# Kernel optimization log

Hardware: AMD Instinct MI355X
Metric: run time of the kernel (lower is better)

## Reference

```python
import jax, jax.numpy as jnp
import numpy as np

B, T, W, D = 4, 1000, 32, 200
ED, N, DCONV, DTR = 400, 16, 4, 13  # d_inner=2*d_model, d_state, d_conv, dt_rank=ceil(200/16)


def _causal_conv(x, w, b):
    # x: (B, L, ED), depthwise causal conv, kernel DCONV
    L = x.shape[1]
    xp = jnp.pad(x, ((0, 0), (DCONV - 1, 0), (0, 0)))
    y = sum(xp[:, k:k + L, :] * w[:, k] for k in range(DCONV))
    return y + b


def _ssm(x, A_log, Dp, xproj, dtw, dtb):
    # selective scan; x: (B, L, ED)
    A = -jnp.exp(A_log)                      # (ED, N)
    dbc = x @ xproj                          # (B, L, DTR+2N)
    delta, Bm, Cm = dbc[..., :DTR], dbc[..., DTR:DTR + N], dbc[..., DTR + N:]
    dt = jax.nn.softplus(delta @ dtw + dtb)  # (B, L, ED)
    dA = jnp.exp(dt[..., None] * A)                         # (B, L, ED, N)
    dBx = dt[..., None] * Bm[:, :, None, :] * x[..., None]  # (B, L, ED, N)

    def step(h, t):
        dA_t, dBx_t, C_t = t
        h = dA_t * h + dBx_t
        y = jnp.einsum('ben,bn->be', h, C_t)
        return h, y

    h0 = jnp.zeros((x.shape[0], ED, N), x.dtype)
    xs = (dA.transpose(1, 0, 2, 3), dBx.transpose(1, 0, 2, 3), Cm.transpose(1, 0, 2))
    _, ys = jax.lax.scan(step, h0, xs)
    return ys.transpose(1, 0, 2) + Dp * x


def _branch(x, in_proj, conv_w, conv_b, xproj, dtw, dtb, A_log, Dp):
    xz = x @ in_proj
    xp, z = xz[..., :ED], xz[..., ED:]
    xp = jax.nn.silu(_causal_conv(xp, conv_w, conv_b))
    y = _ssm(xp, A_log, Dp, xproj, dtw, dtb)
    return y * jax.nn.silu(z)


def setup_inputs() -> dict:
    key = jax.random.key(0)
    ks = jax.random.split(key, 24)
    s = 0.02
    nrm = lambda k, shape: jax.random.normal(k, shape, jnp.float32) * s
    inp = {}
    inp['input_ids'] = jax.random.normal(ks[0], (B, T, W, D), jnp.float32)
    inp['n_tweets'] = jax.random.randint(ks[1], (B,), 1, T + 1)
    inp['n_words'] = jax.random.randint(ks[2], (B, T), 1, W + 1)
    inp['cls_token'] = jnp.zeros((1, 1, D), jnp.float32)
    inp['w_attn'] = nrm(ks[3], (D, 1))
    inp['b_attn'] = jnp.zeros((1,), jnp.float32)
    inp['norm_w'] = jnp.ones((D,), jnp.float32)
    for i, d in enumerate(('f', 'b')):
        o = i * 8
        inp[f'in_proj_{d}'] = nrm(ks[4 + o], (D, 2 * ED))
        inp[f'conv_w_{d}'] = nrm(ks[5 + o], (ED, DCONV))
        inp[f'conv_b_{d}'] = jnp.zeros((ED,), jnp.float32)
        inp[f'xproj_{d}'] = nrm(ks[6 + o], (ED, DTR + 2 * N))
        inp[f'dtw_{d}'] = nrm(ks[7 + o], (DTR, ED))
        inp[f'dtb_{d}'] = jnp.zeros((ED,), jnp.float32)
        inp[f'A_log_{d}'] = jnp.log(jnp.broadcast_to(jnp.arange(1, N + 1, dtype=jnp.float32), (ED, N)))
        inp[f'D_{d}'] = jnp.ones((ED,), jnp.float32)
    inp['out_proj'] = nrm(ks[20], (ED, D))
    inp['head_w'] = nrm(ks[21], (D, 1))
    inp['head_b'] = jnp.zeros((1,), jnp.float32)
    return inp


def reference(input_ids, n_tweets, n_words, cls_token, w_attn, b_attn, norm_w,
              in_proj_f, conv_w_f, conv_b_f, xproj_f, dtw_f, dtb_f, A_log_f, D_f,
              in_proj_b, conv_w_b, conv_b_b, xproj_b, dtw_b, dtb_b, A_log_b, D_b,
              out_proj, head_w, head_b):
    Bz, Tz, Wz, Dz = input_ids.shape
    # ragged per-tweet attention pooling, fully vectorized with masks
    scores = jnp.squeeze(input_ids @ w_attn, -1) + b_attn[0]        # (B, T, W)
    wmask = jnp.arange(Wz) < n_words[..., None]                     # (B, T, W)
    scores = jnp.where(wmask, scores, -jnp.inf)
    attn = jax.nn.softmax(scores, axis=-1)
    tw = jnp.einsum('btw,btwd->btd', attn, input_ids)               # (B, T, D)
    tmask = jnp.arange(Tz) < n_tweets[:, None]
    tw = jnp.where(tmask[..., None], tw, 0.0)                       # padded tweets stay zero
    pos = Tz // 2
    x = jnp.concatenate([tw[:, :pos], jnp.broadcast_to(cls_token, (Bz, 1, Dz)), tw[:, pos:]], axis=1)
    # one bidirectional Mamba layer: pre-RMSNorm residual block
    xn = x * jax.lax.rsqrt(jnp.mean(x * x, axis=-1, keepdims=True) + 1e-5) * norm_w
    y_f = _branch(xn, in_proj_f, conv_w_f, conv_b_f, xproj_f, dtw_f, dtb_f, A_log_f, D_f)
    y_b = jnp.flip(_branch(jnp.flip(xn, 1), in_proj_b, conv_w_b, conv_b_b, xproj_b, dtw_b, dtb_b, A_log_b, D_b), 1)
    x = x + (y_f + y_b) @ out_proj
    logit = jnp.squeeze(x[:, pos] @ head_w, -1) + head_b[0]
    return jax.nn.sigmoid(logit)
```

## Files before the change

kernel.cpp:

```cpp
#include <hip/hip_runtime.h>
#include <cmath>

#define Bz 4
#define Tz 1000
#define Wz 32
#define Dz 200
#define EDz 400
#define Nz 16
#define DTRz 13
#define Lz 1001
#define POSz 500
#define LPz 501
#define TSTR 512
#define ESP 10
#define NEG_BIG -1e30f

__device__ __forceinline__ float wave_sum(float v) {
#pragma unroll
  for (int o = 32; o; o >>= 1) v += __shfl_xor(v, o);
  return v;
}

__global__ __launch_bounds__(256) void k_front(
    const float* __restrict__ x, const int* __restrict__ n_tweets,
    const int* __restrict__ n_words, const float* __restrict__ w_attn,
    const float* __restrict__ b_attn, const float* __restrict__ norm_w,
    const float* __restrict__ cls, const float* __restrict__ out_proj,
    const float* __restrict__ head_w, const float* __restrict__ ipf,
    const float* __restrict__ ipb, float* __restrict__ xn,
    float* __restrict__ zbuf, float* __restrict__ vbuf) {
  int bid = blockIdx.x;
  int tid = threadIdx.x;
  int wave = tid >> 6, lane = tid & 63;
  if (bid < 9) {
    if (bid == 0) {
      __shared__ float hw[Dz];
      if (tid < Dz) hw[tid] = head_w[tid];
      __syncthreads();
      for (int e = tid; e < EDz; e += 256) {
        float acc = 0.f;
        for (int d = 0; d < Dz; d += 4) {
          float4 ov = *(const float4*)(out_proj + e * Dz + d);
          acc += ov.x * hw[d] + ov.y * hw[d + 1] + ov.z * hw[d + 2] + ov.w * hw[d + 3];
        }
        vbuf[e] = acc;
      }
      return;
    }
    int id = bid - 1;
    int br = id >> 2, b = id & 3;
    __shared__ float xs[Dz];
    __shared__ float s_red[4];
    float val = (tid < Dz) ? cls[tid] : 0.f;
    float sq = wave_sum(val * val);
    if ((tid & 63) == 0) s_red[tid >> 6] = sq;
    __syncthreads();
    float tot = s_red[0] + s_red[1] + s_red[2] + s_red[3];
    float scale = rsqrtf(tot * (1.f / Dz) + 1e-5f);
    if (tid < Dz) {
      float o = val * scale * norm_w[tid];
      xs[tid] = o;
      if (br == 0) xn[((size_t)b * Lz + POSz) * Dz + tid] = o;
    }
    __syncthreads();
    const float* ip = br ? ipb : ipf;
    for (int e = tid; e < EDz; e += 256) {
      float acc = 0.f;
      for (int d = 0; d < Dz; ++d) acc += xs[d] * ip[d * (2 * EDz) + EDz + e];
      zbuf[((size_t)br * Bz + b) * EDz + e] = acc;
    }
    return;
  }
  int bt = (bid - 9) * 4 + wave;
  int b = bt / Tz, t = bt - b * Tz;
  int l = (t < POSz) ? t : t + 1;
  float* outr = xn + ((size_t)b * Lz + l) * Dz;
  int ntw = n_tweets[b]; if (ntw > Tz) ntw = Tz;
  if (t >= ntw) {
    if (lane < 50) *(float4*)(outr + lane * 4) = make_float4(0.f, 0.f, 0.f, 0.f);
    return;
  }
  int nw = n_words[b * Tz + t]; if (nw > Wz) nw = Wz; if (nw < 1) nw = 1;
  const float* xs = x + ((size_t)(b * Tz + t)) * (Wz * Dz);
  int h = lane & 1, w = lane >> 1;
  float sc = 0.f;
  if (w < nw) {
    const float* xr = xs + w * Dz + h * 100;
    const float* wr = w_attn + h * 100;
#pragma unroll
    for (int i = 0; i < 25; ++i) {
      float4 xv = *(const float4*)(xr + i * 4);
      float4 wv = *(const float4*)(wr + i * 4);
      sc += xv.x * wv.x + xv.y * wv.y + xv.z * wv.z + xv.w * wv.w;
    }
  }
  sc += __shfl_xor(sc, 1);
  float scv = (w < nw) ? (sc + b_attn[0]) : NEG_BIG;
  float m = scv;
#pragma unroll
  for (int o = 32; o; o >>= 1) m = fmaxf(m, __shfl_xor(m, o));
  float en = __expf(scv - m);
  float es = (h == 0) ? en : 0.f;
  float tot = wave_sum(es);
  en /= tot;
  float4 val = make_float4(0.f, 0.f, 0.f, 0.f);
  const float* xc = xs + lane * 4;
  for (int ww = 0; ww < nw; ++ww) {
    float aw = __shfl(en, 2 * ww);
    if (lane < 50) {
      float4 xv = *(const float4*)(xc + ww * Dz);
      val.x += aw * xv.x; val.y += aw * xv.y;
      val.z += aw * xv.z; val.w += aw * xv.w;
    }
  }
  float sq = (lane < 50) ? (val.x * val.x + val.y * val.y + val.z * val.z + val.w * val.w) : 0.f;
  sq = wave_sum(sq);
  float scale = rsqrtf(sq * (1.f / Dz) + 1e-5f);
  if (lane < 50) {
    float4 nw4 = *(const float4*)(norm_w + lane * 4);
    float4 o = make_float4(val.x * scale * nw4.x, val.y * scale * nw4.y,
                           val.z * scale * nw4.z, val.w * scale * nw4.w);
    *(float4*)(outr + lane * 4) = o;
  }
}

__global__ __launch_bounds__(256) void k_gemm(
    const float* __restrict__ xn, const float* __restrict__ ipf,
    const float* __restrict__ ipb, float* __restrict__ P) {
  int bid = blockIdx.x;
  int brb = bid / 56;
  int rr = bid - brb * 56;
  int tt = rr / 7, ee = rr - tt * 7;
  int br = brb >> 2, b = brb & 3;
  int t0 = tt * 64, e0 = ee * 64;
  const float* ip = br ? ipb : ipf;
  int tid = threadIdx.x;
  int tx = tid & 15, ty = tid >> 4;

  __shared__ float Xs[16][64 + 4];
  __shared__ float Ws[16][64 + 4];

  float acc[4][4];
#pragma unroll
  for (int i = 0; i < 4; ++i)
#pragma unroll
    for (int j = 0; j < 4; ++j) acc[i][j] = 0.f;

  int xr = tid >> 2, xc = (tid & 3) * 4;
  int wr = tid >> 4, wc = (tid & 15) * 4;
  int t = t0 + xr;
  bool tok = (t < LPz);
  int l = br ? (Lz - 1 - t) : t;
  const float* xrow = xn + ((size_t)b * Lz + l) * Dz;

  for (int dk = 0; dk < 200; dk += 16) {
    float xv[4], wv[4];
#pragma unroll
    for (int c = 0; c < 4; ++c) {
      int d = dk + xc + c;
      xv[c] = (tok && d < Dz) ? xrow[d] : 0.f;
    }
    int dw = dk + wr;
#pragma unroll
    for (int c = 0; c < 4; ++c) {
      int e = e0 + wc + c;
      wv[c] = (dw < Dz && e < EDz) ? ip[(size_t)dw * (2 * EDz) + e] : 0.f;
    }
    __syncthreads();
#pragma unroll
    for (int c = 0; c < 4; ++c) Xs[xc + c][xr] = xv[c];
#pragma unroll
    for (int c = 0; c < 4; ++c) Ws[wr][wc + c] = wv[c];
    __syncthreads();
#pragma unroll
    for (int k = 0; k < 16; ++k) {
      float4 a4 = *(const float4*)&Xs[k][ty * 4];
      float4 b4 = *(const float4*)&Ws[k][tx * 4];
      float av[4] = {a4.x, a4.y, a4.z, a4.w};
      float bv[4] = {b4.x, b4.y, b4.z, b4.w};
#pragma unroll
      for (int i = 0; i < 4; ++i)
#pragma unroll
        for (int j = 0; j < 4; ++j) acc[i][j] += av[i] * bv[j];
    }
  }
#pragma unroll
  for (int j = 0; j < 4; ++j) {
    int e = e0 + tx * 4 + j;
    if (e < EDz) {
      float4 o = make_float4(acc[0][j], acc[1][j], acc[2][j], acc[3][j]);
      *(float4*)&P[((size_t)brb * EDz + e) * TSTR + t0 + ty * 4] = o;
    }
  }
}

__global__ __launch_bounds__(256) void k_mid(
    const float* __restrict__ P,
    const float* __restrict__ cwf, const float* __restrict__ cwb,
    const float* __restrict__ cbf, const float* __restrict__ cbb,
    const float* __restrict__ xpjf, const float* __restrict__ xpjb,
    float* __restrict__ xp_t, float* __restrict__ dbcp) {
  int bid = blockIdx.x;
  int esp = bid % ESP;
  int rem = bid / ESP;
  int tc = rem & 7, brb = rem >> 3;
  int br = brb >> 2;
  int tid = threadIdx.x;
  int wave = tid >> 6, lane = tid & 63;
  int t = tc * 64 + lane;
  const float* cw = br ? cwb : cwf;
  const float* cb = br ? cbb : cbf;
  const float* xpj = br ? xpjb : xpjf;

  __shared__ float sred[4][64][45];

  float accq[45];
#pragma unroll
  for (int q = 0; q < 45; ++q) accq[q] = 0.f;

  const float* Pb = P + (size_t)brb * EDz * TSTR;
  int e0 = esp * 40 + wave * 10;
#pragma unroll 2
  for (int i = 0; i < 10; ++i) {
    int e = e0 + i;
    const float* pr = Pb + (size_t)e * TSTR;
    float p0 = (t >= 3) ? pr[t - 3] : 0.f;
    float p1 = (t >= 2) ? pr[t - 2] : 0.f;
    float p2 = (t >= 1) ? pr[t - 1] : 0.f;
    float p3 = pr[t];
    float4 c4 = *(const float4*)(cw + e * 4);
    float a = cb[e] + c4.x * p0 + c4.y * p1 + c4.z * p2 + c4.w * p3;
    float sp = a / (1.f + __expf(-a));
    xp_t[((size_t)brb * EDz + e) * TSTR + t] = sp;
    const float* xq = xpj + e * 45;
#pragma unroll
    for (int q = 0; q < 45; ++q) accq[q] += sp * xq[q];
  }
#pragma unroll
  for (int q = 0; q < 45; ++q) sred[wave][lane][q] = accq[q];
  __syncthreads();
  if (wave < 2) {
#pragma unroll
    for (int q = 0; q < 45; ++q)
      sred[wave][lane][q] += sred[wave + 2][lane][q];
  }
  __syncthreads();
  if (wave == 0) {
    float* dp = dbcp + ((size_t)(esp * 8 + brb) * 45) * TSTR + t;
#pragma unroll
    for (int q = 0; q < 45; ++q)
      dp[(size_t)q * TSTR] = sred[0][lane][q] + sred[1][lane][q];
  }
}

__global__ __launch_bounds__(256) void k_dt2(
    const float* __restrict__ dbcp,
    const float* __restrict__ dtwf, const float* __restrict__ dtwb,
    const float* __restrict__ dtbf, const float* __restrict__ dtbb,
    float* __restrict__ dt_t, float* __restrict__ Bm_t,
    float* __restrict__ Cend) {
  int bid = blockIdx.x;
  int egrp = bid % 11;
  int rem = bid / 11;
  int tc = rem & 7, brb = rem >> 3;
  int br = brb >> 2;
  int tid = threadIdx.x;
  int wave = tid >> 6, lane = tid & 63;
  int t = tc * 64 + lane;
  const size_t espstr = (size_t)8 * 45 * TSTR;

  if (egrp == 10) {
    for (int idx = tid; idx < 16 * 64; idx += 256) {
      int n = idx >> 6, tl = idx & 63;
      size_t base = ((size_t)brb * 45 + 13 + n) * TSTR + tc * 64 + tl;
      float s = 0.f;
#pragma unroll
      for (int esp = 0; esp < ESP; ++esp) s += dbcp[base + esp * espstr];
      Bm_t[((size_t)brb * Nz + n) * TSTR + tc * 64 + tl] = s;
    }
    if (tc == 7 && tid < Nz) {
      size_t base = ((size_t)brb * 45 + 29 + tid) * TSTR + POSz;
      float s = 0.f;
#pragma unroll
      for (int esp = 0; esp < ESP; ++esp) s += dbcp[base + esp * espstr];
      Cend[brb * Nz + tid] = s;
    }
    return;
  }

  __shared__ float dfin[DTRz][64];
  for (int idx = tid; idx < DTRz * 64; idx += 256) {
    int q = idx >> 6, tl = idx & 63;
    size_t base = ((size_t)brb * 45 + q) * TSTR + tc * 64 + tl;
    float s = 0.f;
#pragma unroll
    for (int esp = 0; esp < ESP; ++esp) s += dbcp[base + esp * espstr];
    dfin[q][tl] = s;
  }
  __syncthreads();
  const float* dtw = br ? dtwb : dtwf;
  const float* dtb = br ? dtbb : dtbf;
  float dq[DTRz];
#pragma unroll
  for (int q = 0; q < DTRz; ++q) dq[q] = dfin[q][lane];
  int e0 = egrp * 40 + wave * 10;
#pragma unroll 2
  for (int i = 0; i < 10; ++i) {
    int e = e0 + i;
    float s = dtb[e];
#pragma unroll
    for (int q = 0; q < DTRz; ++q) s += dq[q] * dtw[q * EDz + e];
    float dtv = (s > 20.f) ? s : log1pf(__expf(s));
    dt_t[((size_t)brb * EDz + e) * TSTR + t] = dtv;
  }
}

__global__ __launch_bounds__(64) void k_scan(
    const float* __restrict__ xp_t, const float* __restrict__ dt_t,
    const float* __restrict__ Bm_t, const float* __restrict__ Cend,
    const float* __restrict__ Alogf, const float* __restrict__ Alogb,
    const float* __restrict__ Dpf, const float* __restrict__ Dpb,
    const float* __restrict__ zbuf, const float* __restrict__ vbuf,
    float* __restrict__ ybuf) {
  int blk = blockIdx.x;
  int br = blk / (Bz * EDz);
  int rem = blk - br * (Bz * EDz);
  int b = rem / EDz, e = rem - b * EDz;
  int lane = threadIdx.x;
  const float* A_log = br ? Alogb : Alogf;
  const float* Dp = br ? Dpb : Dpf;
  float A[Nz];
  {
    const float4* ap = (const float4*)(A_log + e * Nz);
#pragma unroll
    for (int q = 0; q < 4; ++q) {
      float4 a4 = ap[q];
      A[q * 4 + 0] = -__expf(a4.x); A[q * 4 + 1] = -__expf(a4.y);
      A[q * 4 + 2] = -__expf(a4.z); A[q * 4 + 3] = -__expf(a4.w);
    }
  }
  size_t base = ((size_t)(br * Bz + b) * EDz + e) * TSTR;
  const float* dtp = dt_t + base;
  const float* xpp = xp_t + base;
  const float* bmp = Bm_t + (size_t)(br * Bz + b) * Nz * TSTR;
  float loc = 0.f;
#pragma unroll
  for (int c = 0; c < 8; ++c) {
    int t = c * 64 + lane;
    if (t < LPz) loc += dtp[t];
  }
  float Stot = wave_sum(loc);
  float acc[Nz];
#pragma unroll
  for (int n = 0; n < Nz; ++n) acc[n] = 0.f;
  float carry = 0.f;
  for (int c = 0; c < 8; ++c) {
    int t = c * 64 + lane;
    bool act = t < LPz;
    float dtt = 0.f, xv = 0.f;
    if (act) { dtt = dtp[t]; xv = xpp[t]; }
    float s = dtt;
#pragma unroll
    for (int o = 1; o < 64; o <<= 1) {
      float u = __shfl_up(s, o);
      s += (lane >= o) ? u : 0.f;
    }
    float S = carry + s;
    carry += __shfl(s, 63);
    float wt = dtt * xv;
    float decay = Stot - S;
#pragma unroll
    for (int n = 0; n < Nz; ++n) {
      float bv = 0.f;
      if (act) bv = bmp[n * TSTR + t];
      acc[n] += __expf(A[n] * decay) * wt * bv;
    }
  }
#pragma unroll
  for (int o = 32; o; o >>= 1) {
#pragma unroll
    for (int n = 0; n < Nz; ++n) acc[n] += __shfl_xor(acc[n], o);
  }
  if (lane == 0) {
    float y = Dp[e] * xpp[LPz - 1];
#pragma unroll
    for (int n = 0; n < Nz; ++n) y += Cend[(br * Bz + b) * Nz + n] * acc[n];
    float zz = zbuf[((size_t)br * Bz + b) * EDz + e];
    float sz = zz / (1.f + __expf(-zz));
    ybuf[((size_t)br * Bz + b) * EDz + e] = y * sz * vbuf[e];
  }
}

__global__ __launch_bounds__(256) void k_final(
    const float* __restrict__ cls, const float* __restrict__ head_w,
    const float* __restrict__ head_b, const float* __restrict__ ybuf,
    float* __restrict__ out) {
  int tid = threadIdx.x;
  int b = tid >> 6, lane = tid & 63;
  float acc = 0.f;
  for (int e = lane; e < EDz; e += 64)
    acc += ybuf[(size_t)b * EDz + e] + ybuf[(size_t)(Bz + b) * EDz + e];
  for (int d = lane; d < Dz; d += 64) acc += cls[d] * head_w[d];
  acc = wave_sum(acc);
  if (lane == 0) out[b] = 1.f / (1.f + __expf(-(acc + head_b[0])));
}

extern "C" void kernel_launch(void* const* d_in, const int* in_sizes, int n_in,
                              void* d_out, int out_size, void* d_ws, size_t ws_size,
                              hipStream_t stream) {
  const float* input_ids = (const float*)d_in[0];
  const int* n_tweets = (const int*)d_in[1];
  const int* n_words = (const int*)d_in[2];
  const float* cls = (const float*)d_in[3];
  const float* w_attn = (const float*)d_in[4];
  const float* b_attn = (const float*)d_in[5];
  const float* norm_w = (const float*)d_in[6];
  const float* ip[2] = {(const float*)d_in[7], (const float*)d_in[15]};
  const float* cw[2] = {(const float*)d_in[8], (const float*)d_in[16]};
  const float* cb[2] = {(const float*)d_in[9], (const float*)d_in[17]};
  const float* xpj[2] = {(const float*)d_in[10], (const float*)d_in[18]};
  const float* dtw[2] = {(const float*)d_in[11], (const float*)d_in[19]};
  const float* dtbp[2] = {(const float*)d_in[12], (const float*)d_in[20]};
  const float* Alog[2] = {(const float*)d_in[13], (const float*)d_in[21]};
  const float* Dpp[2] = {(const float*)d_in[14], (const float*)d_in[22]};
  const float* out_proj = (const float*)d_in[23];
  const float* head_w = (const float*)d_in[24];
  const float* head_b = (const float*)d_in[25];
  float* out = (float*)d_out;

  float* ws = (float*)d_ws;
  float* xn = ws;
  float* Pbuf = xn + 800800;
  float* xp_t = Pbuf + 1638400;
  float* dt_t = xp_t + 1638400;
  float* Bm_t = dt_t + 1638400;
  float* dbcp = Bm_t + 65536;
  float* Cend = dbcp + 1843200;
  float* zbuf = Cend + 128;
  float* vbuf = zbuf + 3200;
  float* ybuf = vbuf + 400;

  hipLaunchKernelGGL(k_front, dim3(9 + Bz * Tz / 4), dim3(256), 0, stream,
                     input_ids, n_tweets, n_words, w_attn, b_attn, norm_w,
                     cls, out_proj, head_w, ip[0], ip[1], xn, zbuf, vbuf);
  hipLaunchKernelGGL(k_gemm, dim3(2 * Bz * 8 * 7), dim3(256), 0, stream,
                     xn, ip[0], ip[1], Pbuf);
  hipLaunchKernelGGL(k_mid, dim3(2 * Bz * 8 * ESP), dim3(256), 0, stream,
                     Pbuf, cw[0], cw[1], cb[0], cb[1], xpj[0], xpj[1],
                     xp_t, dbcp);
  hipLaunchKernelGGL(k_dt2, dim3(2 * Bz * 8 * 11), dim3(256), 0, stream,
                     dbcp, dtw[0], dtw[1], dtbp[0], dtbp[1],
                     dt_t, Bm_t, Cend);
  hipLaunchKernelGGL(k_scan, dim3(2 * Bz * EDz), dim3(64), 0, stream,
                     xp_t, dt_t, Bm_t, Cend, Alog[0], Alog[1], Dpp[0], Dpp[1],
                     zbuf, vbuf, ybuf);
  hipLaunchKernelGGL(k_final, dim3(1), dim3(256), 0, stream,
                     cls, head_w, head_b, ybuf, out);
}
```

Measured before the change: 107.4 us.

## Fuse dt projection into mid kernel and final reduction into scan via atomic counters

Removes two kernel launches by using last-block-done atomic counters. The k_dt2 work (reducing the split-E partial dbc, softplus dt projection, Bm and Cend) now runs in whichever k_mid2 block finishes last for its (branch, batch, time-chunk) tile. The k_final head reduction now runs in the last k_scan2 block. This saves launch and sync overhead, but the dt projection is serialised onto 64 tail blocks, each looping over all 400 channels, where it was spread across 704 blocks before, which may lengthen the tail.

```diff
diff --git a/kernel.cpp b/kernel.cpp
--- a/kernel.cpp
+++ b/kernel.cpp
@@ -28,12 +28,14 @@
     const float* __restrict__ cls, const float* __restrict__ out_proj,
     const float* __restrict__ head_w, const float* __restrict__ ipf,
     const float* __restrict__ ipb, float* __restrict__ xn,
-    float* __restrict__ zbuf, float* __restrict__ vbuf) {
+    float* __restrict__ zbuf, float* __restrict__ vbuf,
+    int* __restrict__ cnts) {
   int bid = blockIdx.x;
   int tid = threadIdx.x;
   int wave = tid >> 6, lane = tid & 63;
   if (bid < 9) {
     if (bid == 0) {
+      if (tid < 72) cnts[tid] = 0;
       __shared__ float hw[Dz];
       if (tid < Dz) hw[tid] = head_w[tid];
       __syncthreads();
@@ -194,12 +196,16 @@
   }
 }
 
-__global__ __launch_bounds__(256) void k_mid(
+__global__ __launch_bounds__(256) void k_mid2(
     const float* __restrict__ P,
     const float* __restrict__ cwf, const float* __restrict__ cwb,
     const float* __restrict__ cbf, const float* __restrict__ cbb,
     const float* __restrict__ xpjf, const float* __restrict__ xpjb,
-    float* __restrict__ xp_t, float* __restrict__ dbcp) {
+    const float* __restrict__ dtwf, const float* __restrict__ dtwb,
+    const float* __restrict__ dtbf, const float* __restrict__ dtbb,
+    float* __restrict__ xp_t, float* __restrict__ dbcp,
+    float* __restrict__ dt_t, float* __restrict__ Bm_t,
+    float* __restrict__ Cend, int* __restrict__ cnts) {
   int bid = blockIdx.x;
   int esp = bid % ESP;
   int rem = bid / ESP;
@@ -213,6 +219,8 @@
   const float* xpj = br ? xpjb : xpjf;
 
   __shared__ float sred[4][64][45];
+  __shared__ float dfin[DTRz * 64];
+  __shared__ int s_last;
 
   float accq[45];
 #pragma unroll
@@ -251,62 +259,50 @@
     for (int q = 0; q < 45; ++q)
       dp[(size_t)q * TSTR] = sred[0][lane][q] + sred[1][lane][q];
   }
-}
-
-__global__ __launch_bounds__(256) void k_dt2(
-    const float* __restrict__ dbcp,
-    const float* __restrict__ dtwf, const float* __restrict__ dtwb,
-    const float* __restrict__ dtbf, const float* __restrict__ dtbb,
-    float* __restrict__ dt_t, float* __restrict__ Bm_t,
-    float* __restrict__ Cend) {
-  int bid = blockIdx.x;
-  int egrp = bid % 11;
-  int rem = bid / 11;
-  int tc = rem & 7, brb = rem >> 3;
-  int br = brb >> 2;
-  int tid = threadIdx.x;
-  int wave = tid >> 6, lane = tid & 63;
-  int t = tc * 64 + lane;
+  __syncthreads();
+  __threadfence();
+  if (tid == 0) {
+    int old = atomicAdd(&cnts[brb * 8 + tc], 1);
+    s_last = (old == ESP - 1) ? 1 : 0;
+  }
+  __syncthreads();
+  if (!s_last) return;
+  __threadfence();
+
   const size_t espstr = (size_t)8 * 45 * TSTR;
-
-  if (egrp == 10) {
-    for (int idx = tid; idx < 16 * 64; idx += 256) {
-      int n = idx >> 6, tl = idx & 63;
-      size_t base = ((size_t)brb * 45 + 13 + n) * TSTR + tc * 64 + tl;
-      float s = 0.f;
-#pragma unroll
-      for (int esp = 0; esp < ESP; ++esp) s += dbcp[base + esp * espstr];
-      Bm_t[((size_t)brb * Nz + n) * TSTR + tc * 64 + tl] = s;
-    }
-    if (tc == 7 && tid < Nz) {
-      size_t base = ((size_t)brb * 45 + 29 + tid) * TSTR + POSz;
-      float s = 0.f;
-#pragma unroll
-      for (int esp = 0; esp < ESP; ++esp) s += dbcp[base + esp * espstr];
-      Cend[brb * Nz + tid] = s;
-    }
-    return;
-  }
-
-  __shared__ float dfin[DTRz][64];
   for (int idx = tid; idx < DTRz * 64; idx += 256) {
     int q = idx >> 6, tl = idx & 63;
     size_t base = ((size_t)brb * 45 + q) * TSTR + tc * 64 + tl;
     float s = 0.f;
 #pragma unroll
-    for (int esp = 0; esp < ESP; ++esp) s += dbcp[base + esp * espstr];
-    dfin[q][tl] = s;
+    for (int e2 = 0; e2 < ESP; ++e2) s += dbcp[base + e2 * espstr];
+    dfin[q * 64 + tl] = s;
+  }
+  for (int idx = tid; idx < Nz * 64; idx += 256) {
+    int n = idx >> 6, tl = idx & 63;
+    size_t base = ((size_t)brb * 45 + 13 + n) * TSTR + tc * 64 + tl;
+    float s = 0.f;
+#pragma unroll
+    for (int e2 = 0; e2 < ESP; ++e2) s += dbcp[base + e2 * espstr];
+    Bm_t[((size_t)brb * Nz + n) * TSTR + tc * 64 + tl] = s;
+  }
+  if (tc == 7 && tid < Nz) {
+    size_t base = ((size_t)brb * 45 + 29 + tid) * TSTR + POSz;
+    float s = 0.f;
+#pragma unroll
+    for (int e2 = 0; e2 < ESP; ++e2) s += dbcp[base + e2 * espstr];
+    Cend[brb * Nz + tid] = s;
   }
   __syncthreads();
   const float* dtw = br ? dtwb : dtwf;
   const float* dtb = br ? dtbb : dtbf;
   float dq[DTRz];
 #pragma unroll
-  for (int q = 0; q < DTRz; ++q) dq[q] = dfin[q][lane];
-  int e0 = egrp * 40 + wave * 10;
+  for (int q = 0; q < DTRz; ++q) dq[q] = dfin[q * 64 + lane];
+  int ew0 = wave * 100;
 #pragma unroll 2
-  for (int i = 0; i < 10; ++i) {
-    int e = e0 + i;
+  for (int i = 0; i < 100; ++i) {
+    int e = ew0 + i;
     float s = dtb[e];
 #pragma unroll
     for (int q = 0; q < DTRz; ++q) s += dq[q] * dtw[q * EDz + e];
@@ -315,13 +311,15 @@
   }
 }
 
-__global__ __launch_bounds__(64) void k_scan(
+__global__ __launch_bounds__(64) void k_scan2(
     const float* __restrict__ xp_t, const float* __restrict__ dt_t,
     const float* __restrict__ Bm_t, const float* __restrict__ Cend,
     const float* __restrict__ Alogf, const float* __restrict__ Alogb,
     const float* __restrict__ Dpf, const float* __restrict__ Dpb,
     const float* __restrict__ zbuf, const float* __restrict__ vbuf,
-    float* __restrict__ ybuf) {
+    float* __restrict__ ybuf, const float* __restrict__ cls,
+    const float* __restrict__ head_w, const float* __restrict__ head_b,
+    float* __restrict__ out, int* __restrict__ cnt) {
   int blk = blockIdx.x;
   int br = blk / (Bz * EDz);
   int rem = blk - br * (Bz * EDz);
@@ -389,20 +387,22 @@
     float sz = zz / (1.f + __expf(-zz));
     ybuf[((size_t)br * Bz + b) * EDz + e] = y * sz * vbuf[e];
   }
-}
-
-__global__ __launch_bounds__(256) void k_final(
-    const float* __restrict__ cls, const float* __restrict__ head_w,
-    const float* __restrict__ head_b, const float* __restrict__ ybuf,
-    float* __restrict__ out) {
-  int tid = threadIdx.x;
-  int b = tid >> 6, lane = tid & 63;
-  float acc = 0.f;
-  for (int e = lane; e < EDz; e += 64)
-    acc += ybuf[(size_t)b * EDz + e] + ybuf[(size_t)(Bz + b) * EDz + e];
-  for (int d = lane; d < Dz; d += 64) acc += cls[d] * head_w[d];
-  acc = wave_sum(acc);
-  if (lane == 0) out[b] = 1.f / (1.f + __expf(-(acc + head_b[0])));
+  __threadfence();
+  int old = 0;
+  if (lane == 0) old = atomicAdd(cnt, 1);
+  old = __shfl(old, 0);
+  if (old != 2 * Bz * EDz - 1) return;
+  __threadfence();
+  float ch = 0.f;
+  for (int d = lane; d < Dz; d += 64) ch += cls[d] * head_w[d];
+  ch = wave_sum(ch) + head_b[0];
+  for (int b2 = 0; b2 < Bz; ++b2) {
+    float a2 = 0.f;
+    for (int e2 = lane; e2 < EDz; e2 += 64)
+      a2 += ybuf[(size_t)b2 * EDz + e2] + ybuf[(size_t)(Bz + b2) * EDz + e2];
+    a2 = wave_sum(a2);
+    if (lane == 0) out[b2] = 1.f / (1.f + __expf(-(a2 + ch)));
+  }
 }
 
 extern "C" void kernel_launch(void* const* d_in, const int* in_sizes, int n_in,
@@ -439,21 +439,18 @@
   float* zbuf = Cend + 128;
   float* vbuf = zbuf + 3200;
   float* ybuf = vbuf + 400;
+  int* cnts = (int*)(ybuf + 3200 + 64);
 
   hipLaunchKernelGGL(k_front, dim3(9 + Bz * Tz / 4), dim3(256), 0, stream,
                      input_ids, n_tweets, n_words, w_attn, b_attn, norm_w,
-                     cls, out_proj, head_w, ip[0], ip[1], xn, zbuf, vbuf);
+                     cls, out_proj, head_w, ip[0], ip[1], xn, zbuf, vbuf, cnts);
   hipLaunchKernelGGL(k_gemm, dim3(2 * Bz * 8 * 7), dim3(256), 0, stream,
                      xn, ip[0], ip[1], Pbuf);
-  hipLaunchKernelGGL(k_mid, dim3(2 * Bz * 8 * ESP), dim3(256), 0, stream,
+  hipLaunchKernelGGL(k_mid2, dim3(2 * Bz * 8 * ESP), dim3(256), 0, stream,
                      Pbuf, cw[0], cw[1], cb[0], cb[1], xpj[0], xpj[1],
-                     xp_t, dbcp);
-  hipLaunchKernelGGL(k_dt2, dim3(2 * Bz * 8 * 11), dim3(256), 0, stream,
-                     dbcp, dtw[0], dtw[1], dtbp[0], dtbp[1],
-                     dt_t, Bm_t, Cend);
-  hipLaunchKernelGGL(k_scan, dim3(2 * Bz * EDz), dim3(64), 0, stream,
+                     dtw[0], dtw[1], dtbp[0], dtbp[1],
+                     xp_t, dbcp, dt_t, Bm_t, Cend, cnts);
+  hipLaunchKernelGGL(k_scan2, dim3(2 * Bz * EDz), dim3(64), 0, stream,
                      xp_t, dt_t, Bm_t, Cend, Alog[0], Alog[1], Dpp[0], Dpp[1],
-                     zbuf, vbuf, ybuf);
-  hipLaunchKernelGGL(k_final, dim3(1), dim3(256), 0, stream,
-                     cls, head_w, head_b, ybuf, out);
-}
+                     zbuf, vbuf, ybuf, cls, head_w, head_b, out, cnts + 64);
+}
```

Result: slower. 374.8 us (+249.0%).

## Fuse in_proj GEMM with conv/x_proj and move dt projection into scan

Applied to the files above, without the earlier changes.

Merges the in_proj GEMM with the causal conv, SiLU and x_proj partial-sum stage. Each block computes an 80-row tile that includes an 8-row halo, keeps it in shared memory, and so no longer round-trips the P buffer through global memory. The dt projection and softplus move out of the dt kernel into the scan kernel, which computes them per lane from the reduced delta rows, so the dt_t buffer is never written or read. This removes one launch and a large share of global traffic. In exchange the GEMM recomputes the halo rows, shared memory per block grows (which may lower occupancy), and the scan does extra arithmetic.

```diff
diff --git a/kernel.cpp b/kernel.cpp
--- a/kernel.cpp
+++ b/kernel.cpp
@@ -12,7 +12,7 @@
 #define POSz 500
 #define LPz 501
 #define TSTR 512
-#define ESP 10
+#define NEE 7
 #define NEG_BIG -1e30f
 
 __device__ __forceinline__ float wave_sum(float v) {
@@ -124,117 +124,108 @@
   }
 }
 
-__global__ __launch_bounds__(256) void k_gemm(
-    const float* __restrict__ xn, const float* __restrict__ ipf,
-    const float* __restrict__ ipb, float* __restrict__ P) {
-  int bid = blockIdx.x;
-  int brb = bid / 56;
-  int rr = bid - brb * 56;
-  int tt = rr / 7, ee = rr - tt * 7;
-  int br = brb >> 2, b = brb & 3;
-  int t0 = tt * 64, e0 = ee * 64;
-  const float* ip = br ? ipb : ipf;
-  int tid = threadIdx.x;
-  int tx = tid & 15, ty = tid >> 4;
-
-  __shared__ float Xs[16][64 + 4];
-  __shared__ float Ws[16][64 + 4];
-
-  float acc[4][4];
-#pragma unroll
-  for (int i = 0; i < 4; ++i)
-#pragma unroll
-    for (int j = 0; j < 4; ++j) acc[i][j] = 0.f;
-
-  int xr = tid >> 2, xc = (tid & 3) * 4;
-  int wr = tid >> 4, wc = (tid & 15) * 4;
-  int t = t0 + xr;
-  bool tok = (t < LPz);
-  int l = br ? (Lz - 1 - t) : t;
-  const float* xrow = xn + ((size_t)b * Lz + l) * Dz;
-
-  for (int dk = 0; dk < 200; dk += 16) {
-    float xv[4], wv[4];
-#pragma unroll
-    for (int c = 0; c < 4; ++c) {
-      int d = dk + xc + c;
-      xv[c] = (tok && d < Dz) ? xrow[d] : 0.f;
-    }
-    int dw = dk + wr;
-#pragma unroll
-    for (int c = 0; c < 4; ++c) {
-      int e = e0 + wc + c;
-      wv[c] = (dw < Dz && e < EDz) ? ip[(size_t)dw * (2 * EDz) + e] : 0.f;
-    }
-    __syncthreads();
-#pragma unroll
-    for (int c = 0; c < 4; ++c) Xs[xc + c][xr] = xv[c];
-#pragma unroll
-    for (int c = 0; c < 4; ++c) Ws[wr][wc + c] = wv[c];
-    __syncthreads();
-#pragma unroll
-    for (int k = 0; k < 16; ++k) {
-      float4 a4 = *(const float4*)&Xs[k][ty * 4];
-      float4 b4 = *(const float4*)&Ws[k][tx * 4];
-      float av[4] = {a4.x, a4.y, a4.z, a4.w};
-      float bv[4] = {b4.x, b4.y, b4.z, b4.w};
-#pragma unroll
-      for (int i = 0; i < 4; ++i)
-#pragma unroll
-        for (int j = 0; j < 4; ++j) acc[i][j] += av[i] * bv[j];
-    }
-  }
-#pragma unroll
-  for (int j = 0; j < 4; ++j) {
-    int e = e0 + tx * 4 + j;
-    if (e < EDz) {
-      float4 o = make_float4(acc[0][j], acc[1][j], acc[2][j], acc[3][j]);
-      *(float4*)&P[((size_t)brb * EDz + e) * TSTR + t0 + ty * 4] = o;
-    }
-  }
-}
-
-__global__ __launch_bounds__(256) void k_mid(
-    const float* __restrict__ P,
+__global__ __launch_bounds__(256) void k_gemmid(
+    const float* __restrict__ xn,
+    const float* __restrict__ ipf, const float* __restrict__ ipb,
     const float* __restrict__ cwf, const float* __restrict__ cwb,
     const float* __restrict__ cbf, const float* __restrict__ cbb,
     const float* __restrict__ xpjf, const float* __restrict__ xpjb,
     float* __restrict__ xp_t, float* __restrict__ dbcp) {
   int bid = blockIdx.x;
-  int esp = bid % ESP;
-  int rem = bid / ESP;
-  int tc = rem & 7, brb = rem >> 3;
-  int br = brb >> 2;
+  int ee = bid % NEE;
+  int rem = bid / NEE;
+  int tt = rem & 7, brb = rem >> 3;
+  int br = brb >> 2, b = brb & 3;
+  int t0 = tt * 64, e0 = ee * 64;
   int tid = threadIdx.x;
   int wave = tid >> 6, lane = tid & 63;
-  int t = tc * 64 + lane;
+  const float* ip = br ? ipb : ipf;
   const float* cw = br ? cwb : cwf;
   const float* cb = br ? cbb : cbf;
   const float* xpj = br ? xpjb : xpjf;
 
+  __shared__ float Xs[16][85];
+  __shared__ float Ws[16][68];
+  __shared__ float Pl[80][69];
   __shared__ float sred[4][64][45];
 
+  int tx = tid & 15, ty = tid >> 4;
+  float acc[5][4];
+#pragma unroll
+  for (int i = 0; i < 5; ++i)
+#pragma unroll
+    for (int j = 0; j < 4; ++j) acc[i][j] = 0.f;
+
+  for (int dk = 0; dk < 200; dk += 16) {
+    float xv[5];
+#pragma unroll
+    for (int r = 0; r < 5; ++r) {
+      int trow = r * 16 + ty;
+      int t = t0 - 8 + trow;
+      int d = dk + tx;
+      float v = 0.f;
+      if (t >= 0 && t < LPz && d < Dz) {
+        int l = br ? (Lz - 1 - t) : t;
+        v = xn[((size_t)b * Lz + l) * Dz + d];
+      }
+      xv[r] = v;
+    }
+    int dw = dk + ty;
+    int e4 = e0 + tx * 4;
+    float wv[4];
+#pragma unroll
+    for (int c = 0; c < 4; ++c) {
+      int e = e4 + c;
+      wv[c] = (dw < Dz && e < EDz) ? ip[(size_t)dw * (2 * EDz) + e] : 0.f;
+    }
+    __syncthreads();
+#pragma unroll
+    for (int r = 0; r < 5; ++r) Xs[tx][r * 16 + ty] = xv[r];
+#pragma unroll
+    for (int c = 0; c < 4; ++c) Ws[ty][tx * 4 + c] = wv[c];
+    __syncthreads();
+#pragma unroll
+    for (int k = 0; k < 16; ++k) {
+      float av[5], bv[4];
+#pragma unroll
+      for (int i = 0; i < 5; ++i) av[i] = Xs[k][ty * 5 + i];
+#pragma unroll
+      for (int j = 0; j < 4; ++j) bv[j] = Ws[k][tx * 4 + j];
+#pragma unroll
+      for (int i = 0; i < 5; ++i)
+#pragma unroll
+        for (int j = 0; j < 4; ++j) acc[i][j] += av[i] * bv[j];
+    }
+  }
+  __syncthreads();
+#pragma unroll
+  for (int i = 0; i < 5; ++i)
+#pragma unroll
+    for (int j = 0; j < 4; ++j) Pl[ty * 5 + i][tx * 4 + j] = acc[i][j];
+  __syncthreads();
+
   float accq[45];
 #pragma unroll
   for (int q = 0; q < 45; ++q) accq[q] = 0.f;
-
-  const float* Pb = P + (size_t)brb * EDz * TSTR;
-  int e0 = esp * 40 + wave * 10;
+  int t = t0 + lane;
 #pragma unroll 2
-  for (int i = 0; i < 10; ++i) {
-    int e = e0 + i;
-    const float* pr = Pb + (size_t)e * TSTR;
-    float p0 = (t >= 3) ? pr[t - 3] : 0.f;
-    float p1 = (t >= 2) ? pr[t - 2] : 0.f;
-    float p2 = (t >= 1) ? pr[t - 1] : 0.f;
-    float p3 = pr[t];
-    float4 c4 = *(const float4*)(cw + e * 4);
-    float a = cb[e] + c4.x * p0 + c4.y * p1 + c4.z * p2 + c4.w * p3;
-    float sp = a / (1.f + __expf(-a));
-    xp_t[((size_t)brb * EDz + e) * TSTR + t] = sp;
-    const float* xq = xpj + e * 45;
-#pragma unroll
-    for (int q = 0; q < 45; ++q) accq[q] += sp * xq[q];
+  for (int i = 0; i < 16; ++i) {
+    int e_loc = wave * 16 + i;
+    int e = e0 + e_loc;
+    if (e < EDz) {
+      int row = lane + 8;
+      float p0 = Pl[row - 3][e_loc];
+      float p1 = Pl[row - 2][e_loc];
+      float p2 = Pl[row - 1][e_loc];
+      float p3 = Pl[row][e_loc];
+      float4 c4 = *(const float4*)(cw + e * 4);
+      float a = cb[e] + c4.x * p0 + c4.y * p1 + c4.z * p2 + c4.w * p3;
+      float sp = a / (1.f + __expf(-a));
+      xp_t[((size_t)brb * EDz + e) * TSTR + t] = sp;
+      const float* xq = xpj + e * 45;
+#pragma unroll
+      for (int q = 0; q < 45; ++q) accq[q] += sp * xq[q];
+    }
   }
 #pragma unroll
   for (int q = 0; q < 45; ++q) sred[wave][lane][q] = accq[q];
@@ -246,89 +237,63 @@
   }
   __syncthreads();
   if (wave == 0) {
-    float* dp = dbcp + ((size_t)(esp * 8 + brb) * 45) * TSTR + t;
+    float* dp = dbcp + ((size_t)(ee * 8 + brb) * 45) * TSTR + t;
 #pragma unroll
     for (int q = 0; q < 45; ++q)
       dp[(size_t)q * TSTR] = sred[0][lane][q] + sred[1][lane][q];
   }
 }
 
-__global__ __launch_bounds__(256) void k_dt2(
-    const float* __restrict__ dbcp,
-    const float* __restrict__ dtwf, const float* __restrict__ dtwb,
-    const float* __restrict__ dtbf, const float* __restrict__ dtbb,
-    float* __restrict__ dt_t, float* __restrict__ Bm_t,
-    float* __restrict__ Cend) {
+__global__ __launch_bounds__(256) void k_dt3(
+    const float* __restrict__ dbcp, float* __restrict__ dfin_g,
+    float* __restrict__ Bm_t, float* __restrict__ Cend) {
   int bid = blockIdx.x;
-  int egrp = bid % 11;
-  int rem = bid / 11;
+  int rg = bid & 3;
+  int rem = bid >> 2;
   int tc = rem & 7, brb = rem >> 3;
-  int br = brb >> 2;
   int tid = threadIdx.x;
-  int wave = tid >> 6, lane = tid & 63;
-  int t = tc * 64 + lane;
   const size_t espstr = (size_t)8 * 45 * TSTR;
-
-  if (egrp == 10) {
-    for (int idx = tid; idx < 16 * 64; idx += 256) {
-      int n = idx >> 6, tl = idx & 63;
-      size_t base = ((size_t)brb * 45 + 13 + n) * TSTR + tc * 64 + tl;
-      float s = 0.f;
-#pragma unroll
-      for (int esp = 0; esp < ESP; ++esp) s += dbcp[base + esp * espstr];
-      Bm_t[((size_t)brb * Nz + n) * TSTR + tc * 64 + tl] = s;
-    }
-    if (tc == 7 && tid < Nz) {
-      size_t base = ((size_t)brb * 45 + 29 + tid) * TSTR + POSz;
-      float s = 0.f;
-#pragma unroll
-      for (int esp = 0; esp < ESP; ++esp) s += dbcp[base + esp * espstr];
-      Cend[brb * Nz + tid] = s;
-    }
-    return;
-  }
-
-  __shared__ float dfin[DTRz][64];
-  for (int idx = tid; idx < DTRz * 64; idx += 256) {
-    int q = idx >> 6, tl = idx & 63;
-    size_t base = ((size_t)brb * 45 + q) * TSTR + tc * 64 + tl;
+  int r0 = rg * 8;
+  int nrows = (rg == 3) ? 5 : 8;
+  for (int idx = tid; idx < nrows * 64; idx += 256) {
+    int rl = idx >> 6, tl = idx & 63;
+    int row = r0 + rl;
+    size_t base = ((size_t)brb * 45 + row) * TSTR + tc * 64 + tl;
     float s = 0.f;
 #pragma unroll
-    for (int esp = 0; esp < ESP; ++esp) s += dbcp[base + esp * espstr];
-    dfin[q][tl] = s;
-  }
-  __syncthreads();
-  const float* dtw = br ? dtwb : dtwf;
-  const float* dtb = br ? dtbb : dtbf;
-  float dq[DTRz];
-#pragma unroll
-  for (int q = 0; q < DTRz; ++q) dq[q] = dfin[q][lane];
-  int e0 = egrp * 40 + wave * 10;
-#pragma unroll 2
-  for (int i = 0; i < 10; ++i) {
-    int e = e0 + i;
-    float s = dtb[e];
-#pragma unroll
-    for (int q = 0; q < DTRz; ++q) s += dq[q] * dtw[q * EDz + e];
-    float dtv = (s > 20.f) ? s : log1pf(__expf(s));
-    dt_t[((size_t)brb * EDz + e) * TSTR + t] = dtv;
-  }
-}
-
-__global__ __launch_bounds__(64) void k_scan(
-    const float* __restrict__ xp_t, const float* __restrict__ dt_t,
+    for (int p = 0; p < NEE; ++p) s += dbcp[base + p * espstr];
+    int tg = tc * 64 + tl;
+    if (row < DTRz) dfin_g[((size_t)brb * DTRz + row) * TSTR + tg] = s;
+    else Bm_t[((size_t)brb * Nz + (row - DTRz)) * TSTR + tg] = s;
+  }
+  if (rg == 3 && tc == 7 && tid < Nz) {
+    size_t base = ((size_t)brb * 45 + 29 + tid) * TSTR + POSz;
+    float s = 0.f;
+#pragma unroll
+    for (int p = 0; p < NEE; ++p) s += dbcp[base + p * espstr];
+    Cend[brb * Nz + tid] = s;
+  }
+}
+
+__global__ __launch_bounds__(64) void k_scan3(
+    const float* __restrict__ xp_t, const float* __restrict__ dfin_g,
     const float* __restrict__ Bm_t, const float* __restrict__ Cend,
     const float* __restrict__ Alogf, const float* __restrict__ Alogb,
     const float* __restrict__ Dpf, const float* __restrict__ Dpb,
+    const float* __restrict__ dtwf, const float* __restrict__ dtwb,
+    const float* __restrict__ dtbf, const float* __restrict__ dtbb,
     const float* __restrict__ zbuf, const float* __restrict__ vbuf,
     float* __restrict__ ybuf) {
   int blk = blockIdx.x;
   int br = blk / (Bz * EDz);
   int rem = blk - br * (Bz * EDz);
   int b = rem / EDz, e = rem - b * EDz;
+  int brb = br * Bz + b;
   int lane = threadIdx.x;
   const float* A_log = br ? Alogb : Alogf;
   const float* Dp = br ? Dpb : Dpf;
+  const float* dtw = br ? dtwb : dtwf;
+  const float* dtb = br ? dtbb : dtbf;
   float A[Nz];
   {
     const float4* ap = (const float4*)(A_log + e * Nz);
@@ -339,15 +304,26 @@
       A[q * 4 + 2] = -__expf(a4.z); A[q * 4 + 3] = -__expf(a4.w);
     }
   }
-  size_t base = ((size_t)(br * Bz + b) * EDz + e) * TSTR;
-  const float* dtp = dt_t + base;
-  const float* xpp = xp_t + base;
-  const float* bmp = Bm_t + (size_t)(br * Bz + b) * Nz * TSTR;
+  float wq[DTRz];
+#pragma unroll
+  for (int q = 0; q < DTRz; ++q) wq[q] = dtw[q * EDz + e];
+  float dtbe = dtb[e];
+  const float* dfb = dfin_g + (size_t)brb * DTRz * TSTR;
+  const float* xpp = xp_t + ((size_t)brb * EDz + e) * TSTR;
+  const float* bmp = Bm_t + (size_t)brb * Nz * TSTR;
+
+  float dtt_r[8];
   float loc = 0.f;
 #pragma unroll
   for (int c = 0; c < 8; ++c) {
     int t = c * 64 + lane;
-    if (t < LPz) loc += dtp[t];
+    float s = dtbe;
+#pragma unroll
+    for (int q = 0; q < DTRz; ++q) s += dfb[(size_t)q * TSTR + t] * wq[q];
+    float dtv = (s > 20.f) ? s : log1pf(__expf(s));
+    dtv = (t < LPz) ? dtv : 0.f;
+    dtt_r[c] = dtv;
+    loc += dtv;
   }
   float Stot = wave_sum(loc);
   float acc[Nz];
@@ -357,8 +333,8 @@
   for (int c = 0; c < 8; ++c) {
     int t = c * 64 + lane;
     bool act = t < LPz;
-    float dtt = 0.f, xv = 0.f;
-    if (act) { dtt = dtp[t]; xv = xpp[t]; }
+    float dtt = dtt_r[c];
+    float xv = act ? xpp[t] : 0.f;
     float s = dtt;
 #pragma unroll
     for (int o = 1; o < 64; o <<= 1) {
@@ -371,8 +347,7 @@
     float decay = Stot - S;
 #pragma unroll
     for (int n = 0; n < Nz; ++n) {
-      float bv = 0.f;
-      if (act) bv = bmp[n * TSTR + t];
+      float bv = act ? bmp[n * TSTR + t] : 0.f;
       acc[n] += __expf(A[n] * decay) * wt * bv;
     }
   }
@@ -384,10 +359,10 @@
   if (lane == 0) {
     float y = Dp[e] * xpp[LPz - 1];
 #pragma unroll
-    for (int n = 0; n < Nz; ++n) y += Cend[(br * Bz + b) * Nz + n] * acc[n];
-    float zz = zbuf[((size_t)br * Bz + b) * EDz + e];
+    for (int n = 0; n < Nz; ++n) y += Cend[brb * Nz + n] * acc[n];
+    float zz = zbuf[(size_t)brb * EDz + e];
     float sz = zz / (1.f + __expf(-zz));
-    ybuf[((size_t)br * Bz + b) * EDz + e] = y * sz * vbuf[e];
+    ybuf[(size_t)brb * EDz + e] = y * sz * vbuf[e];
   }
 }
 
@@ -430,12 +405,11 @@
 
   float* ws = (float*)d_ws;
   float* xn = ws;
-  float* Pbuf = xn + 800800;
-  float* xp_t = Pbuf + 1638400;
-  float* dt_t = xp_t + 1638400;
-  float* Bm_t = dt_t + 1638400;
+  float* xp_t = xn + 800800;
+  float* Bm_t = xp_t + 1638400;
   float* dbcp = Bm_t + 65536;
-  float* Cend = dbcp + 1843200;
+  float* dfin = dbcp + 1290240;
+  float* Cend = dfin + 53248;
   float* zbuf = Cend + 128;
   float* vbuf = zbuf + 3200;
   float* ybuf = vbuf + 400;
@@ -443,17 +417,14 @@
   hipLaunchKernelGGL(k_front, dim3(9 + Bz * Tz / 4), dim3(256), 0, stream,
                      input_ids, n_tweets, n_words, w_attn, b_attn, norm_w,
                      cls, out_proj, head_w, ip[0], ip[1], xn, zbuf, vbuf);
-  hipLaunchKernelGGL(k_gemm, dim3(2 * Bz * 8 * 7), dim3(256), 0, stream,
-                     xn, ip[0], ip[1], Pbuf);
-  hipLaunchKernelGGL(k_mid, dim3(2 * Bz * 8 * ESP), dim3(256), 0, stream,
-                     Pbuf, cw[0], cw[1], cb[0], cb[1], xpj[0], xpj[1],
-                     xp_t, dbcp);
-  hipLaunchKernelGGL(k_dt2, dim3(2 * Bz * 8 * 11), dim3(256), 0, stream,
-                     dbcp, dtw[0], dtw[1], dtbp[0], dtbp[1],
-                     dt_t, Bm_t, Cend);
-  hipLaunchKernelGGL(k_scan, dim3(2 * Bz * EDz), dim3(64), 0, stream,
-                     xp_t, dt_t, Bm_t, Cend, Alog[0], Alog[1], Dpp[0], Dpp[1],
-                     zbuf, vbuf, ybuf);
+  hipLaunchKernelGGL(k_gemmid, dim3(2 * Bz * 8 * NEE), dim3(256), 0, stream,
+                     xn, ip[0], ip[1], cw[0], cw[1], cb[0], cb[1],
+                     xpj[0], xpj[1], xp_t, dbcp);
+  hipLaunchKernelGGL(k_dt3, dim3(2 * Bz * 8 * 4), dim3(256), 0, stream,
+                     dbcp, dfin, Bm_t, Cend);
+  hipLaunchKernelGGL(k_scan3, dim3(2 * Bz * EDz), dim3(64), 0, stream,
+                     xp_t, dfin, Bm_t, Cend, Alog[0], Alog[1], Dpp[0], Dpp[1],
+                     dtw[0], dtw[1], dtbp[0], dtbp[1], zbuf, vbuf, ybuf);
   hipLaunchKernelGGL(k_final, dim3(1), dim3(256), 0, stream,
                      cls, head_w, head_b, ybuf, out);
 }
```

Result: faster. 97.66 us (-9.1%).
